# Performance work log

Measured on AMD Instinct MI355X. Metric: run time of the kernel, lower is better.

## Reference

```python
import jax, jax.numpy as jnp
import numpy as np

N = 100000      # nodes
E = 3200000     # edges (avg degree 32)
F_IN = 512      # input features
H = 16          # hidden (module default)
C = 40          # classes


def _linear_params(key, fan_in, fan_out):
    # torch.nn.Linear default init: U(-1/sqrt(fan_in), 1/sqrt(fan_in))
    k1, k2 = jax.random.split(key)
    lim = 1.0 / np.sqrt(fan_in)
    W = jax.random.uniform(k1, (fan_in, fan_out), jnp.float32, -lim, lim)
    b = jax.random.uniform(k2, (fan_out,), jnp.float32, -lim, lim)
    return W, b


def setup_inputs() -> dict:
    key = jax.random.key(0)
    ks = jax.random.split(key, 8)
    x = jax.random.normal(ks[0], (N, F_IN), jnp.float32)
    edge_index = jax.random.randint(ks[1], (2, E), 0, N, dtype=jnp.int64)
    edge_weight = jax.random.uniform(ks[2], (E,), jnp.float32)
    W_first, b_first = _linear_params(ks[3], F_IN, H)
    W_conv1, b_conv1 = _linear_params(ks[4], H, H)
    W_conv2, b_conv2 = _linear_params(ks[5], H, H)
    W_out, b_out = _linear_params(ks[6], H, C)
    return {
        "x": x, "edge_index": edge_index, "edge_weight": edge_weight,
        "W_first": W_first, "b_first": b_first,
        "W_conv1": W_conv1, "b_conv1": b_conv1,
        "W_conv2": W_conv2, "b_conv2": b_conv2,
        "W_out": W_out, "b_out": b_out,
    }


def _gcn_conv(x, W, b, row, col, ew):
    # PyG GCNConv: h = x @ W; out_i = sum_{(j->i)} norm_e * h_j + b
    # norm_e = deg^-1/2[row] * w_e * deg^-1/2[col], deg from target (col) index,
    # with self-loops (weight 1) already appended to row/col/ew.
    n = x.shape[0]
    deg = jax.ops.segment_sum(ew, col, num_segments=n)
    dinv = jnp.where(deg > 0, jax.lax.rsqrt(deg), 0.0)
    norm = dinv[row] * ew * dinv[col]
    h = x @ W
    out = jax.ops.segment_sum(h[row] * norm[:, None], col, num_segments=n)
    return out + b


def reference(x, edge_index, edge_weight, W_first, b_first,
              W_conv1, b_conv1, W_conv2, b_conv2, W_out, b_out):
    n = x.shape[0]
    # add self-loops once (shared by all conv layers)
    loop = jnp.arange(n, dtype=edge_index.dtype)
    row = jnp.concatenate([edge_index[0], loop])
    col = jnp.concatenate([edge_index[1], loop])
    ew = jnp.concatenate([edge_weight, jnp.ones((n,), edge_weight.dtype)])

    h = jax.nn.relu(x @ W_first + b_first)
    # dropout: eval mode -> identity
    h = jax.nn.relu(_gcn_conv(h, W_conv1, b_conv1, row, col, ew))
    h = jax.nn.relu(_gcn_conv(h, W_conv2, b_conv2, row, col, ew))
    # dropout: eval mode -> identity
    logits = h @ W_out + b_out
    return jax.nn.log_softmax(logits, axis=-1)
```

## Files before the change

### kernel.cpp

```cpp
#include <hip/hip_runtime.h>
#include <hip/hip_bf16.h>
#include <hip/hip_fp16.h>
#include <math.h>

#define F_IN 512
#define H 16
#define BSH 7
#define BNODES (1 << BSH)
#define SSH 12
#define EPT 64
#define CAP 5376
#define SEG 4096
#define SL 33


__global__ __launch_bounds__(256) void hist_kernel(const int* __restrict__ col,
                                                   int* __restrict__ bcnt, int E, int NBUCK) {
    extern __shared__ int hs[];
    const int t = threadIdx.x;
    for (int i = t; i < NBUCK; i += 256) hs[i] = 0;
    __syncthreads();
    long long e0 = (long long)blockIdx.x * (256 * EPT) + t;
#pragma unroll 4
    for (int k = 0; k < EPT; ++k) {
        long long e = e0 + (long long)k * 256;
        if (e < E) atomicAdd(&hs[col[e] >> BSH], 1);
    }
    __syncthreads();
    for (int i = t; i < NBUCK; i += 256) {
        int h = hs[i];
        if (h > 0) atomicAdd(&bcnt[i], h);
    }
}

__global__ void bscan_kernel(const int* __restrict__ bcnt, int* __restrict__ bbase,
                             int* __restrict__ sbase, int* __restrict__ rowptr,
                             int NBUCK, int nsup, int E, int N) {
    __shared__ int sm[1024];
    int t = threadIdx.x;
    int v = (t < NBUCK) ? bcnt[t] : 0;
    sm[t] = v;
    __syncthreads();
    for (int o = 1; o < 1024; o <<= 1) {
        int u = (t >= o) ? sm[t - o] : 0;
        __syncthreads();
        sm[t] += u;
        __syncthreads();
    }
    if (t < NBUCK) bbase[t] = sm[t] - v;
    if (t == 0) { bbase[NBUCK] = E; rowptr[N] = E; }
    __syncthreads();
    if (t < nsup) {
        int bk = t << (SSH - BSH);
        sbase[t] = (bk < NBUCK) ? (sm[bk] - bcnt[bk]) : E;
    }
    if (t == nsup) sbase[nsup] = E;
}


__global__ __launch_bounds__(256) void scat1_kernel(const int* __restrict__ row,
                                                    const int* __restrict__ col,
                                                    const float* __restrict__ ew,
                                                    const int* __restrict__ sbase,
                                                    int* __restrict__ sfill,
                                                    int2* __restrict__ ptmp, int E, int nsup) {
    __shared__ int2 stg[SEG];
    __shared__ unsigned char sup[SEG];
    __shared__ int cnt[32], base[32];
    const int t = threadIdx.x;
    const int e0 = blockIdx.x * SEG;
    int m = E - e0; if (m > SEG) m = SEG;
    if (t < 32) cnt[t] = 0;
    __syncthreads();
    for (int i = t; i < m; i += 256) {
        int e = e0 + i;
        int c = col[e];
        int s = c >> SSH;
        sup[i] = (unsigned char)s;
        atomicAdd(&cnt[s], 1);
        stg[i] = make_int2(row[e] | ((c & ((1 << SSH) - 1)) << 17), __float_as_int(ew[e]));
    }
    __syncthreads();
    if (t < nsup) {
        int h = cnt[t];
        base[t] = h ? atomicAdd(&sfill[t], h) : 0;
        cnt[t] = 0;
    }
    __syncthreads();
    for (int i = t; i < m; i += 256) {
        int s = sup[i];
        int rk = atomicAdd(&cnt[s], 1);
        ptmp[sbase[s] + base[s] + rk] = stg[i];
    }
}


__global__ __launch_bounds__(256) void scat2_kernel(const int* __restrict__ sbase,
                                                    const int* __restrict__ bbase,
                                                    int* __restrict__ ffill,
                                                    const int2* __restrict__ ptmp,
                                                    int2* __restrict__ packed, int NBUCK) {
    __shared__ int2 stg[SEG];
    __shared__ int cnt[32], base[32];
    const int t = threadIdx.x;
    const int s  = blockIdx.x / SL;
    const int sl = blockIdx.x % SL;
    const int ss = sbase[s];
    const int len = sbase[s + 1] - ss;
    const int lo = ss + (int)((long long)len * sl / SL);
    const int hi = ss + (int)((long long)len * (sl + 1) / SL);
    int m = hi - lo; if (m > SEG) m = SEG;
    if (t < 32) cnt[t] = 0;
    __syncthreads();
    for (int i = t; i < m; i += 256) {
        int2 p = ptmp[lo + i];
        stg[i] = p;
        int bk5 = ((unsigned)p.x >> (17 + BSH)) & 31;
        atomicAdd(&cnt[bk5], 1);
    }
    __syncthreads();
    if (t < 32) {
        int bk = (s << 5) + t;
        int h = cnt[t];
        base[t] = (h && bk < NBUCK) ? atomicAdd(&ffill[bk], h) : 0;
        cnt[t] = 0;
    }
    __syncthreads();
    for (int i = t; i < m; i += 256) {
        int2 p = stg[i];
        int bk5 = ((unsigned)p.x >> (17 + BSH)) & 31;
        int rk = atomicAdd(&cnt[bk5], 1);
        int bk = (s << 5) + bk5;
        packed[bbase[bk] + base[bk5] + rk] = make_int2(p.x & 0xFFFFFF, p.y);
    }
}

__global__ __launch_bounds__(256) void pass2_kernel(const int* __restrict__ bbase,
                                                    int2* __restrict__ packed,
                                                    int* __restrict__ rowptr,
                                                    float* __restrict__ dinv, int N) {
    __shared__ int2  edg[CAP];
    __shared__ int   ncnt[BNODES], nsc[BNODES], nfill[BNODES];
    __shared__ float dsum[BNODES];
    const int t = threadIdx.x;
    const int b = blockIdx.x;
    const int s = bbase[b];
    int cnt = bbase[b + 1] - s;
    if (cnt > CAP) cnt = CAP;

    for (int i = t; i < cnt; i += 256) edg[i] = packed[s + i];
    if (t < BNODES) { ncnt[t] = 0; nfill[t] = 0; dsum[t] = 0.f; }
    __syncthreads();

    for (int i = t; i < cnt; i += 256) {
        int lc = (edg[i].x >> 17) & (BNODES - 1);
        atomicAdd(&ncnt[lc], 1);
        atomicAdd(&dsum[lc], __int_as_float(edg[i].y));
    }
    __syncthreads();
    if (t < BNODES) nsc[t] = ncnt[t];
    __syncthreads();
    for (int o = 1; o < BNODES; o <<= 1) {
        int v = (t < BNODES && t >= o) ? nsc[t - o] : 0;
        __syncthreads();
        if (t < BNODES) nsc[t] += v;
        __syncthreads();
    }
    if (t < BNODES) {
        int n = b * BNODES + t;
        if (n < N) {
            rowptr[n] = s + nsc[t] - ncnt[t];
            dinv[n]   = rsqrtf(1.0f + dsum[t]);
        }
    }
    __syncthreads();
    for (int i = t; i < cnt; i += 256) {
        int lc = (edg[i].x >> 17) & (BNODES - 1);
        int rk = atomicAdd(&nfill[lc], 1);
        packed[s + nsc[lc] - ncnt[lc] + rk] = make_int2(edg[i].x & 0x1FFFF, edg[i].y);
    }
}


#define L1_ROWS 8
#define XS_CH 20

__global__ __launch_bounds__(256) void l1_kernel(const float* __restrict__ x,
                                                 const float* __restrict__ W,
                                                 const float* __restrict__ b,
                                                 float* __restrict__ h0, int N) {
    __shared__ float  xs[L1_ROWS][32 * XS_CH];
    __shared__ float2 part[L1_ROWS][256];
    const int t  = threadIdx.x;
    const int o  = t & 7;
    const int fg = t >> 3;

    float w0[16], w1[16];
#pragma unroll
    for (int j = 0; j < 16; ++j) {
        w0[j] = W[(fg * 16 + j) * H + o];
        w1[j] = W[(fg * 16 + j) * H + o + 8];
    }

    const int nbatch = (N + L1_ROWS - 1) / L1_ROWS;
    for (int batch = blockIdx.x; batch < nbatch; batch += gridDim.x) {
        const int row0 = batch * L1_ROWS;
#pragma unroll
        for (int bq = 0; bq < 4; ++bq) {
            int L  = bq * 256 + t;
            int rl = L >> 7;
            int f4 = L & 127;
            int r  = row0 + rl;
            float4 v = make_float4(0.f, 0.f, 0.f, 0.f);
            if (r < N) v = *(const float4*)&x[(size_t)r * F_IN + f4 * 4];
            int c = f4 >> 2, j4 = f4 & 3;
            *(float4*)&xs[rl][c * XS_CH + j4 * 4] = v;
        }
        __syncthreads();

        float acc0[L1_ROWS], acc1[L1_ROWS];
#pragma unroll
        for (int r = 0; r < L1_ROWS; ++r) { acc0[r] = 0.f; acc1[r] = 0.f; }
#pragma unroll
        for (int j4 = 0; j4 < 4; ++j4) {
#pragma unroll
            for (int r = 0; r < L1_ROWS; ++r) {
                float4 xv = *(const float4*)&xs[r][fg * XS_CH + j4 * 4];
                acc0[r] = fmaf(xv.x, w0[j4 * 4 + 0], acc0[r]);
                acc0[r] = fmaf(xv.y, w0[j4 * 4 + 1], acc0[r]);
                acc0[r] = fmaf(xv.z, w0[j4 * 4 + 2], acc0[r]);
                acc0[r] = fmaf(xv.w, w0[j4 * 4 + 3], acc0[r]);
                acc1[r] = fmaf(xv.x, w1[j4 * 4 + 0], acc1[r]);
                acc1[r] = fmaf(xv.y, w1[j4 * 4 + 1], acc1[r]);
                acc1[r] = fmaf(xv.z, w1[j4 * 4 + 2], acc1[r]);
                acc1[r] = fmaf(xv.w, w1[j4 * 4 + 3], acc1[r]);
            }
        }
#pragma unroll
        for (int r = 0; r < L1_ROWS; ++r) part[r][fg * 8 + o] = make_float2(acc0[r], acc1[r]);
        __syncthreads();

        if (t < 128) {
            int r = t >> 4, oo = t & 15;
            int o8 = oo & 7;
            float s = 0.f;
#pragma unroll
            for (int g = 0; g < 32; ++g) {
                float2 p = part[r][g * 8 + o8];
                s += (oo < 8) ? p.x : p.y;
            }
            s = fmaxf(s + b[oo], 0.f);
            int rr = row0 + r;
            if (rr < N) h0[(size_t)rr * H + oo] = s;
        }
        __syncthreads();
    }
}


__global__ __launch_bounds__(256) void mm16_kernel(const float* __restrict__ hin,
                                                   const float* __restrict__ W,
                                                   const float* __restrict__ dinv,
                                                   __half* __restrict__ hWs, int N) {
    __shared__ float Wl[H * H];
    if (threadIdx.x < H * H) Wl[threadIdx.x] = W[threadIdx.x];
    __syncthreads();
    int n = blockIdx.x * 256 + threadIdx.x;
    if (n >= N) return;
    float hv[H];
#pragma unroll
    for (int k4 = 0; k4 < 4; ++k4) {
        float4 v = *(const float4*)&hin[(size_t)n * H + k4 * 4];
        hv[k4 * 4 + 0] = v.x; hv[k4 * 4 + 1] = v.y;
        hv[k4 * 4 + 2] = v.z; hv[k4 * 4 + 3] = v.w;
    }
    float acc[H];
#pragma unroll
    for (int c = 0; c < H; ++c) acc[c] = 0.f;
#pragma unroll
    for (int k = 0; k < H; ++k) {
#pragma unroll
        for (int c = 0; c < H; ++c) acc[c] = fmaf(hv[k], Wl[k * H + c], acc[c]);
    }
    float di = dinv[n];
    __half2 hp[8];
#pragma unroll
    for (int i = 0; i < 8; ++i)
        hp[i] = __half2(__float2half(di * acc[2 * i]), __float2half(di * acc[2 * i + 1]));
    *(uint4*)&hWs[(size_t)n * H]     = *(uint4*)&hp[0];
    *(uint4*)&hWs[(size_t)n * H + 8] = *(uint4*)&hp[4];
}


__global__ __launch_bounds__(256) void gather_kernel(const int* __restrict__ rowptr,
                                                     const int2* __restrict__ packed,
                                                     const __half* __restrict__ hWs,
                                                     const float* __restrict__ dinv,
                                                     const float* __restrict__ b,
                                                     float* __restrict__ out, int N) {
    int t = blockIdx.x * 256 + threadIdx.x;
    int n = t >> 4, f = t & 15;
    if (n >= N) return;
    int s = rowptr[n], e = rowptr[n + 1];
    float acc = __half2float(hWs[(size_t)n * H + f]);
    int i = s;
    for (; i + 2 <= e; i += 2) {
        int2 p0 = packed[i], p1 = packed[i + 1];
        float h0 = __half2float(hWs[(size_t)p0.x * H + f]);
        float h1 = __half2float(hWs[(size_t)p1.x * H + f]);
        acc = fmaf(__int_as_float(p0.y), h0, acc);
        acc = fmaf(__int_as_float(p1.y), h1, acc);
    }
    if (i < e) {
        int2 p = packed[i];
        acc = fmaf(__int_as_float(p.y), __half2float(hWs[(size_t)p.x * H + f]), acc);
    }
    out[(size_t)n * H + f] = fmaxf(fmaf(dinv[n], acc, b[f]), 0.f);
}


__global__ __launch_bounds__(256) void out_kernel(const float* __restrict__ h,
                                                  const float* __restrict__ W,
                                                  const float* __restrict__ b,
                                                  float* __restrict__ out, int N, int C) {
    extern __shared__ float sm[];
    float* Wl = sm;
    float* bl = sm + H * C;
    for (int i = threadIdx.x; i < H * C; i += 256) Wl[i] = W[i];
    if (threadIdx.x < C) bl[threadIdx.x] = b[threadIdx.x];
    __syncthreads();
    int n = blockIdx.x * 256 + threadIdx.x;
    if (n >= N) return;
    float hv[H];
#pragma unroll
    for (int k4 = 0; k4 < 4; ++k4) {
        float4 v = *(const float4*)&h[(size_t)n * H + k4 * 4];
        hv[k4 * 4 + 0] = v.x; hv[k4 * 4 + 1] = v.y;
        hv[k4 * 4 + 2] = v.z; hv[k4 * 4 + 3] = v.w;
    }
    float acc[40];
    for (int c = 0; c < C; ++c) acc[c] = bl[c];
    for (int k = 0; k < H; ++k) {
        float xk = hv[k];
        for (int c = 0; c < C; ++c) acc[c] = fmaf(xk, Wl[k * C + c], acc[c]);
    }
    float m = -1e30f;
    for (int c = 0; c < C; ++c) m = fmaxf(m, acc[c]);
    float s = 0.f;
    for (int c = 0; c < C; ++c) s += __expf(acc[c] - m);
    float lse = m + __logf(s);
    for (int c = 0; c < C; ++c) acc[c] -= lse;
    for (int c4 = 0; c4 < C / 4; ++c4) {
        float4 v = make_float4(acc[c4 * 4], acc[c4 * 4 + 1], acc[c4 * 4 + 2], acc[c4 * 4 + 3]);
        *(float4*)&out[(size_t)n * C + c4 * 4] = v;
    }
}


extern "C" void kernel_launch(void* const* d_in, const int* in_sizes, int n_in,
                              void* d_out, int out_size, void* d_ws, size_t ws_size,
                              hipStream_t stream) {
    const float* x       = (const float*)d_in[0];
    const int*   ei      = (const int*)d_in[1];
    const float* ew      = (const float*)d_in[2];
    const float* W_first = (const float*)d_in[3];
    const float* b_first = (const float*)d_in[4];
    const float* W_c1    = (const float*)d_in[5];
    const float* b_c1    = (const float*)d_in[6];
    const float* W_c2    = (const float*)d_in[7];
    const float* b_c2    = (const float*)d_in[8];
    const float* W_o     = (const float*)d_in[9];
    const float* b_o     = (const float*)d_in[10];

    const int N = in_sizes[0] / F_IN;
    const int E = in_sizes[2];
    const int C = in_sizes[10];
    const int NBUCK = (N + BNODES - 1) >> BSH;
    const int NSUP  = ((N - 1) >> SSH) + 1;
    const int HB    = (E + 256 * EPT - 1) / (256 * EPT);
    const int SB    = (E + SEG - 1) / SEG;

    const int* row = ei;
    const int* col = ei + E;

    char* wsb = (char*)d_ws;
    int*   bcnt   = (int*)wsb;                  wsb += (size_t)NBUCK * 4;
    int*   sfill  = (int*)wsb;                  wsb += (size_t)32 * 4;
    int*   ffill  = (int*)wsb;                  wsb += (size_t)NBUCK * 4;
    int*   bbase  = (int*)wsb;                  wsb += (size_t)(NBUCK + 1) * 4;
    int*   sbase  = (int*)wsb;                  wsb += (size_t)(NSUP + 1) * 4;
    int*   rowptr = (int*)wsb;                  wsb += (size_t)(N + 1) * 4;
    float* dinv   = (float*)wsb;                wsb += (size_t)N * 4;
    int2*  packed = (int2*)wsb;                 wsb += (size_t)E * 8;
    int2*  ptmp   = (int2*)wsb;                 wsb += (size_t)E * 8;
    float*  bufA  = (float*)ptmp;
    __half* bufB  = (__half*)d_out;

    hipMemsetAsync(bcnt, 0, (size_t)(NBUCK * 2 + 32) * 4, stream);

    hist_kernel<<<HB, 256, NBUCK * 4, stream>>>(col, bcnt, E, NBUCK);
    bscan_kernel<<<1, 1024, 0, stream>>>(bcnt, bbase, sbase, rowptr, NBUCK, NSUP, E, N);
    scat1_kernel<<<SB, 256, 0, stream>>>(row, col, ew, sbase, sfill, ptmp, E, NSUP);
    scat2_kernel<<<NSUP * SL, 256, 0, stream>>>(sbase, bbase, ffill, ptmp, packed, NBUCK);
    pass2_kernel<<<NBUCK, 256, 0, stream>>>(bbase, packed, rowptr, dinv, N);

    l1_kernel<<<1024, 256, 0, stream>>>(x, W_first, b_first, bufA, N);

    mm16_kernel<<<(N + 255) / 256, 256, 0, stream>>>(bufA, W_c1, dinv, bufB, N);
    gather_kernel<<<(N * 16 + 255) / 256, 256, 0, stream>>>(rowptr, packed, bufB, dinv, b_c1, bufA, N);

    mm16_kernel<<<(N + 255) / 256, 256, 0, stream>>>(bufA, W_c2, dinv, bufB, N);
    gather_kernel<<<(N * 16 + 255) / 256, 256, 0, stream>>>(rowptr, packed, bufB, dinv, b_c2, bufA, N);

    size_t smem = (size_t)(H * C + C) * sizeof(float);
    out_kernel<<<(N + 255) / 256, 256, smem, stream>>>(bufA, W_o, b_o, (float*)d_out, N, C);
}
```

Baseline: 696.3 us.

## Replace CSR build with fixed-capacity bucket layout and shared-memory atomic gather

Drops the per-bucket histogram/scan and the per-node CSR sort pass. Edges are scattered into fixed-capacity (CAP) slots per 128-node bucket, and degree sums come from a lighter degsum kernel. The gather now runs one block per bucket, staging edges in LDS and accumulating with shared-memory float atomics instead of using per-node CSR rows. This removes a full pass over the edge array plus the scan, at the cost of LDS atomic contention in the gather and silently truncating buckets that exceed CAP.

```diff
diff --git a/kernel.cpp b/kernel.cpp
--- a/kernel.cpp
+++ b/kernel.cpp
@@ -12,48 +12,42 @@
 #define CAP 5376
 #define SEG 4096
 #define SL 33
-
-
-__global__ __launch_bounds__(256) void hist_kernel(const int* __restrict__ col,
-                                                   int* __restrict__ bcnt, int E, int NBUCK) {
-    extern __shared__ int hs[];
+#define GSTG 2048
+
+
+__global__ __launch_bounds__(256) void hist25_kernel(const int* __restrict__ col,
+                                                     int* __restrict__ scnt, int E) {
+    __shared__ int hs[32];
     const int t = threadIdx.x;
-    for (int i = t; i < NBUCK; i += 256) hs[i] = 0;
+    if (t < 32) hs[t] = 0;
     __syncthreads();
     long long e0 = (long long)blockIdx.x * (256 * EPT) + t;
 #pragma unroll 4
     for (int k = 0; k < EPT; ++k) {
         long long e = e0 + (long long)k * 256;
-        if (e < E) atomicAdd(&hs[col[e] >> BSH], 1);
-    }
-    __syncthreads();
-    for (int i = t; i < NBUCK; i += 256) {
-        int h = hs[i];
-        if (h > 0) atomicAdd(&bcnt[i], h);
-    }
-}
-
-__global__ void bscan_kernel(const int* __restrict__ bcnt, int* __restrict__ bbase,
-                             int* __restrict__ sbase, int* __restrict__ rowptr,
-                             int NBUCK, int nsup, int E, int N) {
-    __shared__ int sm[1024];
+        if (e < E) atomicAdd(&hs[col[e] >> SSH], 1);
+    }
+    __syncthreads();
+    if (t < 32) {
+        int h = hs[t];
+        if (h > 0) atomicAdd(&scnt[t], h);
+    }
+}
+
+__global__ void sscan_kernel(const int* __restrict__ scnt, int* __restrict__ sbase,
+                             int nsup, int E) {
+    __shared__ int sm[64];
     int t = threadIdx.x;
-    int v = (t < NBUCK) ? bcnt[t] : 0;
+    int v = (t < nsup) ? scnt[t] : 0;
     sm[t] = v;
     __syncthreads();
-    for (int o = 1; o < 1024; o <<= 1) {
+    for (int o = 1; o < 64; o <<= 1) {
         int u = (t >= o) ? sm[t - o] : 0;
         __syncthreads();
         sm[t] += u;
         __syncthreads();
     }
-    if (t < NBUCK) bbase[t] = sm[t] - v;
-    if (t == 0) { bbase[NBUCK] = E; rowptr[N] = E; }
-    __syncthreads();
-    if (t < nsup) {
-        int bk = t << (SSH - BSH);
-        sbase[t] = (bk < NBUCK) ? (sm[bk] - bcnt[bk]) : E;
-    }
+    if (t < nsup) sbase[t] = sm[t] - v;
     if (t == nsup) sbase[nsup] = E;
 }
 
@@ -96,7 +90,6 @@
 
 
 __global__ __launch_bounds__(256) void scat2_kernel(const int* __restrict__ sbase,
-                                                    const int* __restrict__ bbase,
                                                     int* __restrict__ ffill,
                                                     const int2* __restrict__ ptmp,
                                                     int2* __restrict__ packed, int NBUCK) {
@@ -131,53 +124,30 @@
         int bk5 = ((unsigned)p.x >> (17 + BSH)) & 31;
         int rk = atomicAdd(&cnt[bk5], 1);
         int bk = (s << 5) + bk5;
-        packed[bbase[bk] + base[bk5] + rk] = make_int2(p.x & 0xFFFFFF, p.y);
-    }
-}
-
-__global__ __launch_bounds__(256) void pass2_kernel(const int* __restrict__ bbase,
-                                                    int2* __restrict__ packed,
-                                                    int* __restrict__ rowptr,
-                                                    float* __restrict__ dinv, int N) {
-    __shared__ int2  edg[CAP];
-    __shared__ int   ncnt[BNODES], nsc[BNODES], nfill[BNODES];
+        int off = base[bk5] + rk;
+        if (off < CAP)
+            packed[(size_t)bk * CAP + off] = make_int2(p.x & 0xFFFFFF, p.y);
+    }
+}
+
+
+__global__ __launch_bounds__(256) void degsum_kernel(const int* __restrict__ ffill,
+                                                     const int2* __restrict__ packed,
+                                                     float* __restrict__ dinv, int N) {
     __shared__ float dsum[BNODES];
-    const int t = threadIdx.x;
-    const int b = blockIdx.x;
-    const int s = bbase[b];
-    int cnt = bbase[b + 1] - s;
-    if (cnt > CAP) cnt = CAP;
-
-    for (int i = t; i < cnt; i += 256) edg[i] = packed[s + i];
-    if (t < BNODES) { ncnt[t] = 0; nfill[t] = 0; dsum[t] = 0.f; }
-    __syncthreads();
-
+    const int t = threadIdx.x, bk = blockIdx.x;
+    int cnt = ffill[bk]; if (cnt > CAP) cnt = CAP;
+    const size_t base = (size_t)bk * CAP;
+    if (t < BNODES) dsum[t] = 0.f;
+    __syncthreads();
     for (int i = t; i < cnt; i += 256) {
-        int lc = (edg[i].x >> 17) & (BNODES - 1);
-        atomicAdd(&ncnt[lc], 1);
-        atomicAdd(&dsum[lc], __int_as_float(edg[i].y));
-    }
-    __syncthreads();
-    if (t < BNODES) nsc[t] = ncnt[t];
-    __syncthreads();
-    for (int o = 1; o < BNODES; o <<= 1) {
-        int v = (t < BNODES && t >= o) ? nsc[t - o] : 0;
-        __syncthreads();
-        if (t < BNODES) nsc[t] += v;
-        __syncthreads();
-    }
+        int2 p = packed[base + i];
+        atomicAdd(&dsum[(p.x >> 17) & (BNODES - 1)], __int_as_float(p.y));
+    }
+    __syncthreads();
     if (t < BNODES) {
-        int n = b * BNODES + t;
-        if (n < N) {
-            rowptr[n] = s + nsc[t] - ncnt[t];
-            dinv[n]   = rsqrtf(1.0f + dsum[t]);
-        }
-    }
-    __syncthreads();
-    for (int i = t; i < cnt; i += 256) {
-        int lc = (edg[i].x >> 17) & (BNODES - 1);
-        int rk = atomicAdd(&nfill[lc], 1);
-        packed[s + nsc[lc] - ncnt[lc] + rk] = make_int2(edg[i].x & 0x1FFFF, edg[i].y);
+        int n = bk * BNODES + t;
+        if (n < N) dinv[n] = rsqrtf(1.0f + dsum[t]);
     }
 }
 
@@ -292,30 +262,41 @@
 }
 
 
-__global__ __launch_bounds__(256) void gather_kernel(const int* __restrict__ rowptr,
-                                                     const int2* __restrict__ packed,
-                                                     const __half* __restrict__ hWs,
-                                                     const float* __restrict__ dinv,
-                                                     const float* __restrict__ b,
-                                                     float* __restrict__ out, int N) {
-    int t = blockIdx.x * 256 + threadIdx.x;
-    int n = t >> 4, f = t & 15;
-    if (n >= N) return;
-    int s = rowptr[n], e = rowptr[n + 1];
-    float acc = __half2float(hWs[(size_t)n * H + f]);
-    int i = s;
-    for (; i + 2 <= e; i += 2) {
-        int2 p0 = packed[i], p1 = packed[i + 1];
-        float h0 = __half2float(hWs[(size_t)p0.x * H + f]);
-        float h1 = __half2float(hWs[(size_t)p1.x * H + f]);
-        acc = fmaf(__int_as_float(p0.y), h0, acc);
-        acc = fmaf(__int_as_float(p1.y), h1, acc);
-    }
-    if (i < e) {
-        int2 p = packed[i];
-        acc = fmaf(__int_as_float(p.y), __half2float(hWs[(size_t)p.x * H + f]), acc);
-    }
-    out[(size_t)n * H + f] = fmaxf(fmaf(dinv[n], acc, b[f]), 0.f);
+__global__ __launch_bounds__(256) void bgather_kernel(const int* __restrict__ ffill,
+                                                      const int2* __restrict__ packed,
+                                                      const __half* __restrict__ hWs,
+                                                      const float* __restrict__ dinv,
+                                                      const float* __restrict__ b,
+                                                      float* __restrict__ out, int N) {
+    __shared__ float acc[BNODES * H];
+    __shared__ int2  stg[GSTG];
+    const int t = threadIdx.x, bk = blockIdx.x;
+    int cnt = ffill[bk]; if (cnt > CAP) cnt = CAP;
+    const size_t base = (size_t)bk * CAP;
+    for (int i = t; i < BNODES * H; i += 256) acc[i] = 0.f;
+    __syncthreads();
+    const int f = t & 15;
+    for (int c0 = 0; c0 < cnt; c0 += GSTG) {
+        int m = cnt - c0; if (m > GSTG) m = GSTG;
+        for (int i = t; i < m; i += 256) stg[i] = packed[base + c0 + i];
+        __syncthreads();
+        for (int i = t >> 4; i < m; i += 16) {
+            int2 p = stg[i];
+            int r  = p.x & 0x1FFFF;
+            int lc = (p.x >> 17) & (BNODES - 1);
+            float h = __half2float(hWs[(size_t)r * H + f]);
+            atomicAdd(&acc[lc * H + f], __int_as_float(p.y) * h);
+        }
+        __syncthreads();
+    }
+    for (int i = t; i < BNODES * H; i += 256) {
+        int n = bk * BNODES + (i >> 4);
+        if (n < N) {
+            int ff = i & 15;
+            float self = __half2float(hWs[(size_t)n * H + ff]);
+            out[(size_t)n * H + ff] = fmaxf(fmaf(dinv[n], acc[i] + self, b[ff]), 0.f);
+        }
+    }
 }
 
 
@@ -384,33 +365,31 @@
     const int* col = ei + E;
 
     char* wsb = (char*)d_ws;
-    int*   bcnt   = (int*)wsb;                  wsb += (size_t)NBUCK * 4;
+    int*   scnt   = (int*)wsb;                  wsb += (size_t)32 * 4;
     int*   sfill  = (int*)wsb;                  wsb += (size_t)32 * 4;
     int*   ffill  = (int*)wsb;                  wsb += (size_t)NBUCK * 4;
-    int*   bbase  = (int*)wsb;                  wsb += (size_t)(NBUCK + 1) * 4;
     int*   sbase  = (int*)wsb;                  wsb += (size_t)(NSUP + 1) * 4;
-    int*   rowptr = (int*)wsb;                  wsb += (size_t)(N + 1) * 4;
     float* dinv   = (float*)wsb;                wsb += (size_t)N * 4;
-    int2*  packed = (int2*)wsb;                 wsb += (size_t)E * 8;
+    int2*  packed = (int2*)wsb;                 wsb += (size_t)NBUCK * CAP * 8;
     int2*  ptmp   = (int2*)wsb;                 wsb += (size_t)E * 8;
     float*  bufA  = (float*)ptmp;
     __half* bufB  = (__half*)d_out;
 
-    hipMemsetAsync(bcnt, 0, (size_t)(NBUCK * 2 + 32) * 4, stream);
-
-    hist_kernel<<<HB, 256, NBUCK * 4, stream>>>(col, bcnt, E, NBUCK);
-    bscan_kernel<<<1, 1024, 0, stream>>>(bcnt, bbase, sbase, rowptr, NBUCK, NSUP, E, N);
+    hipMemsetAsync(scnt, 0, (size_t)(64 + NBUCK) * 4, stream);
+
+    hist25_kernel<<<HB, 256, 0, stream>>>(col, scnt, E);
+    sscan_kernel<<<1, 64, 0, stream>>>(scnt, sbase, NSUP, E);
     scat1_kernel<<<SB, 256, 0, stream>>>(row, col, ew, sbase, sfill, ptmp, E, NSUP);
-    scat2_kernel<<<NSUP * SL, 256, 0, stream>>>(sbase, bbase, ffill, ptmp, packed, NBUCK);
-    pass2_kernel<<<NBUCK, 256, 0, stream>>>(bbase, packed, rowptr, dinv, N);
+    scat2_kernel<<<NSUP * SL, 256, 0, stream>>>(sbase, ffill, ptmp, packed, NBUCK);
+    degsum_kernel<<<NBUCK, 256, 0, stream>>>(ffill, packed, dinv, N);
 
     l1_kernel<<<1024, 256, 0, stream>>>(x, W_first, b_first, bufA, N);
 
     mm16_kernel<<<(N + 255) / 256, 256, 0, stream>>>(bufA, W_c1, dinv, bufB, N);
-    gather_kernel<<<(N * 16 + 255) / 256, 256, 0, stream>>>(rowptr, packed, bufB, dinv, b_c1, bufA, N);
+    bgather_kernel<<<NBUCK, 256, 0, stream>>>(ffill, packed, bufB, dinv, b_c1, bufA, N);
 
     mm16_kernel<<<(N + 255) / 256, 256, 0, stream>>>(bufA, W_c2, dinv, bufB, N);
-    gather_kernel<<<(N * 16 + 255) / 256, 256, 0, stream>>>(rowptr, packed, bufB, dinv, b_c2, bufA, N);
+    bgather_kernel<<<NBUCK, 256, 0, stream>>>(ffill, packed, bufB, dinv, b_c2, bufA, N);
 
     size_t smem = (size_t)(H * C + C) * sizeof(float);
     out_kernel<<<(N + 255) / 256, 256, smem, stream>>>(bufA, W_o, b_o, (float*)d_out, N, C);
```

Result: slower. 1.259 ms (+80.8%).
